# Optimization experiments

Measured on AMD Instinct MI355X. Metric: run time of the kernel, lower is better.

Reference implementation:

```python
import jax, jax.numpy as jnp
import numpy as np

B, C_IN, C_OUT, H, W, K = 8, 64, 64, 64, 64, 9
T = H * W  # 4096 tokens
EPS = 1e-12  # F.normalize eps


def setup_inputs() -> dict:
    key = jax.random.key(0)
    ks = jax.random.split(key, 7)
    x = jax.random.normal(ks[0], (B, C_IN, H, W), dtype=jnp.float32)
    Wq = jax.random.normal(ks[1], (T, T), dtype=jnp.float32) * 0.02
    Wk = jax.random.normal(ks[2], (T, T), dtype=jnp.float32) * 0.02
    Wv = jax.random.normal(ks[3], (T, T), dtype=jnp.float32) * 0.02
    Wo = jax.random.normal(ks[4], (T, T), dtype=jnp.float32) * 0.02
    conv_w = jax.random.normal(ks[5], (C_OUT, C_IN, K), dtype=jnp.float32) * 0.05
    conv_b = jax.random.normal(ks[6], (C_OUT,), dtype=jnp.float32) * 0.01
    return {"x": x, "Wq": Wq, "Wk": Wk, "Wv": Wv, "Wo": Wo,
            "conv_w": conv_w, "conv_b": conv_b}


def reference(x, Wq, Wk, Wv, Wo, conv_w, conv_b):
    Bq, Cc, Hh, Ww = x.shape
    Tt = Hh * Ww
    xf = x.reshape(Bq, Cc, Tt)  # flatten(start_dim=2)
    # nn.Linear over the token (last) dim: y[...,s] = sum_t x[...,t] * W[s,t]
    q = jnp.einsum('bct,st->bcs', xf, Wq)
    k = jnp.einsum('bct,st->bcs', xf, Wk)
    v = jnp.einsum('bct,st->bcs', xf, Wv)
    # cosine similarity over channel dim (dim=1), clamp to >= 0
    kn = k / jnp.maximum(jnp.linalg.norm(k, axis=1, keepdims=True), EPS)
    qn = q / jnp.maximum(jnp.linalg.norm(q, axis=1, keepdims=True), EPS)
    sim = jnp.clip(jnp.einsum('bct,bcs->bts', kn, qn), 0.0, None)  # [B,T,T]
    # top-K most similar neighbors per token (largest=True for similarity)
    _, idx = jax.lax.top_k(sim, K)  # [B,T,K] int32
    # gather neighbor values: prime[b,c,t,j] = v[b,c,idx[b,t,j]]
    gather = jax.vmap(lambda vv, ii: vv[:, ii])  # vv:[C,T], ii:[T,K] -> [C,T,K]
    prime = gather(v, idx).reshape(Bq, Cc, Tt * K)
    # Conv1d(kernel=K, stride=K, padding=0): aggregates each K-neighbor group
    out = jax.lax.conv_general_dilated(
        prime, conv_w, window_strides=(K,), padding='VALID',
        dimension_numbers=('NCH', 'OIH', 'NCH'))  # [B,C_OUT,T]
    out = out + conv_b[None, :, None]
    out = jnp.einsum('bct,st->bcs', out, Wo)  # w_o over token dim
    return out.reshape(Bq, conv_w.shape[0], Hh, Ww)
```

## Files before the change

kernel.cpp:

```cpp
#include <hip/hip_runtime.h>

#define T4096 4096
#define CH 64
typedef unsigned long long u64;

__global__ __launch_bounds__(512) void gemm_qkv(
    const float* __restrict__ X,
    const float* __restrict__ Wq, const float* __restrict__ Wk, const float* __restrict__ Wv,
    float* __restrict__ QT, float* __restrict__ KT, float* __restrict__ VT)
{
    const float* W = (blockIdx.z == 0) ? Wq : (blockIdx.z == 1) ? Wk : Wv;
    float*       O = (blockIdx.z == 0) ? QT : (blockIdx.z == 1) ? KT : VT;
    const int b  = blockIdx.y;
    const int s0 = blockIdx.x * 128;

    __shared__ float As[64][132];
    __shared__ float Bs[64][68];

    const int tid = threadIdx.x;
    const int tx = tid & 15;   const int c0 = tx * 4;
    const int my = tid >> 4;   const int m0 = my * 4;
    const int lr = tid >> 3;
    const int lk = (tid & 7) * 4;
    const int sw = lk;

    float acc[4][4];
#pragma unroll
    for (int i = 0; i < 4; ++i)
#pragma unroll
        for (int j = 0; j < 4; ++j) acc[i][j] = 0.f;

    const float* Xb = X + (size_t)b * CH * T4096;

    for (int k0 = 0; k0 < T4096; k0 += 64) {
#pragma unroll
        for (int kk = 0; kk < 2; ++kk) {
            const int kb = 32 * kk + lk;
#pragma unroll
            for (int p = 0; p < 2; ++p) {
                int row = lr + 64 * p;
                float4 v = *(const float4*)(W + (size_t)(s0 + row) * T4096 + k0 + kb);
                int col = row ^ sw;
                As[kb + 0][col] = v.x; As[kb + 1][col] = v.y;
                As[kb + 2][col] = v.z; As[kb + 3][col] = v.w;
            }
            {
                int row = lr;
                float4 v = *(const float4*)(Xb + (size_t)row * T4096 + k0 + kb);
                int col = row ^ sw;
                Bs[kb + 0][col] = v.x; Bs[kb + 1][col] = v.y;
                Bs[kb + 2][col] = v.z; Bs[kb + 3][col] = v.w;
            }
        }
        __syncthreads();
#pragma unroll
        for (int k = 0; k < 64; ++k) {
            const int swk = k & 28;
            float4 a  = *(const float4*)&As[k][m0 ^ swk];
            float4 bv = *(const float4*)&Bs[k][c0 ^ swk];
            float am[4] = {a.x, a.y, a.z, a.w};
            float bn[4] = {bv.x, bv.y, bv.z, bv.w};
#pragma unroll
            for (int i = 0; i < 4; ++i)
#pragma unroll
                for (int j = 0; j < 4; ++j) acc[i][j] = fmaf(am[i], bn[j], acc[i][j]);
        }
        __syncthreads();
    }
    if (blockIdx.z == 0) {
#pragma unroll
        for (int i = 0; i < 4; ++i) {
            int s = s0 + m0 + i;
            *(float4*)(O + ((((size_t)b * 64 + (s >> 6)) * 16 + tx) * 64 + (s & 63)) * 4) =
                make_float4(acc[i][0], acc[i][1], acc[i][2], acc[i][3]);
        }
    } else {
#pragma unroll
        for (int i = 0; i < 4; ++i) {
            *(float4*)(O + ((size_t)b * T4096 + s0 + m0 + i) * CH + c0) =
                make_float4(acc[i][0], acc[i][1], acc[i][2], acc[i][3]);
        }
    }
}

__global__ __launch_bounds__(256) void normalize_qk(float* __restrict__ QT, float* __restrict__ KT)
{
    int gtok = blockIdx.x * 4 + (threadIdx.x >> 6);
    int lane = threadIdx.x & 63;
    bool isQ = (gtok < 8 * T4096);
    int t = gtok & (T4096 - 1);
    int b = (gtok >> 12) & 7;
    float* p;
    if (isQ) p = QT + ((((size_t)b * 64 + (t >> 6)) * 16 + (lane >> 2)) * 64 + (t & 63)) * 4 + (lane & 3);
    else     p = KT + ((size_t)b * T4096 + t) * CH + lane;
    float v = *p;
    float ss = v * v;
#pragma unroll
    for (int off = 32; off; off >>= 1) ss += __shfl_xor(ss, off);
    float n = fmaxf(sqrtf(ss), 1e-12f);
    *p = v / n;
}

__global__ __launch_bounds__(512) void sim_topk(
    const float* __restrict__ Qr, const float* __restrict__ KT, int* __restrict__ IDX)
{
    const int wg = blockIdx.x;
    const int b  = wg & 7;
    const int t0 = (wg >> 3) * 32;

    __shared__ float Kn[32][68];

    const int tid = threadIdx.x;
    const int tx = tid & 31;
    const int ty = tid >> 5;

    {
        int row = tid >> 4; int cc = (tid & 15) * 4;
        *(float4*)&Kn[row][cc] =
            *(const float4*)(KT + ((size_t)b * T4096 + t0 + row) * CH + cc);
    }
    __syncthreads();

    u64 tv[2][9];
#pragma unroll
    for (int r = 0; r < 2; ++r)
#pragma unroll
        for (int q = 0; q < 9; ++q) tv[r][q] = 0ULL;
    u64 thr[2] = {0ULL, 0ULL};
    unsigned thr_hi[2] = {0u, 0u};

    const float* qb0 = Qr + ((size_t)b * 64 * 1024 + tx) * 4;

    for (int it = 0; it < 16; ++it) {
        const float* bp = qb0 + (size_t)(it * 4) * 4096;
        float acc[2][8];
#pragma unroll
        for (int c = 0; c < 8; ++c) { acc[0][c] = 0.f; acc[1][c] = 0.f; }

#pragma unroll 1
        for (int c4g = 0; c4g < 16; ++c4g) {
            float4 qv[8];
#pragma unroll
            for (int cc = 0; cc < 8; ++cc)
                qv[cc] = *(const float4*)(bp + (size_t)(cc >> 1) * 4096
                                             + c4g * 256 + (cc & 1) * 128);
            float4 k0 = *(const float4*)&Kn[ty][c4g * 4];
            float4 k1 = *(const float4*)&Kn[16 + ty][c4g * 4];
#pragma unroll
            for (int cc = 0; cc < 8; ++cc) {
                acc[0][cc] = fmaf(k0.x, qv[cc].x, acc[0][cc]);
                acc[0][cc] = fmaf(k0.y, qv[cc].y, acc[0][cc]);
                acc[0][cc] = fmaf(k0.z, qv[cc].z, acc[0][cc]);
                acc[0][cc] = fmaf(k0.w, qv[cc].w, acc[0][cc]);
                acc[1][cc] = fmaf(k1.x, qv[cc].x, acc[1][cc]);
                acc[1][cc] = fmaf(k1.y, qv[cc].y, acc[1][cc]);
                acc[1][cc] = fmaf(k1.z, qv[cc].z, acc[1][cc]);
                acc[1][cc] = fmaf(k1.w, qv[cc].w, acc[1][cc]);
            }
        }

        bool ins = false;
        const int sb = it * 256 + tx;
#pragma unroll
        for (int rr = 0; rr < 2; ++rr)
#pragma unroll
            for (int cc = 0; cc < 8; ++cc) {
                float v = fmaxf(acc[rr][cc], 0.f);
                unsigned vb = __float_as_uint(v);
                if (vb >= thr_hi[rr]) {
                    int s = sb + 32 * cc;
                    u64 key = ((u64)vb << 32) | (u64)(4095 - s);
                    if (key > thr[rr]) {
                        u64 cv = key;
#pragma unroll
                        for (int p = 0; p < 9; ++p) {
                            u64 t  = tv[rr][p];
                            bool g = cv > t;
                            tv[rr][p] = g ? cv : t;
                            cv        = g ? t  : cv;
                        }
                        ins = true;
                    }
                }
            }
        if (__any(ins)) {
#pragma unroll
            for (int r = 0; r < 2; ++r) {
                u64 m = tv[r][8];
#pragma unroll
                for (int msk = 1; msk < 32; msk <<= 1) {
                    u64 o = __shfl_xor(m, msk);
                    if (o > m) m = o;
                }
                thr[r] = m;
                thr_hi[r] = (unsigned)(m >> 32);
            }
        }
    }

#pragma unroll
    for (int rr = 0; rr < 2; ++rr) {
        u64 mv[9];
#pragma unroll
        for (int q = 0; q < 9; ++q) mv[q] = tv[rr][q];
        const int outrow = t0 + rr * 16 + ty;
        int* dst = IDX + ((size_t)b * T4096 + outrow) * 9;
        for (int sel = 0; sel < 9; ++sel) {
            u64 bk = mv[0]; int bl = tx;
#pragma unroll
            for (int m = 1; m < 32; m <<= 1) {
                u64 ok = __shfl_xor(bk, m);
                int ol = __shfl_xor(bl, m);
                if (ok > bk) { bk = ok; bl = ol; }
            }
            if (tx == 0) dst[sel] = 4095 - (int)(unsigned)bk;
            if (tx == bl) {
#pragma unroll
                for (int q = 0; q < 8; ++q) mv[q] = mv[q + 1];
                mv[8] = 0ULL;
            }
        }
    }
}

__global__ void transpose_w(const float* __restrict__ cw, float* __restrict__ wT3)
{
    int idx = blockIdx.x * 256 + threadIdx.x;
    if (idx >= 64 * 64 * 9) return;
    int q   = idx & 3;
    int o   = (idx >> 2) & 63;
    int i4g = (idx >> 8) & 15;
    int j   = idx >> 12;
    wT3[idx] = cw[o * 576 + (i4g * 4 + q) * 9 + j];
}

__global__ __launch_bounds__(256) void gather_conv(
    const float* __restrict__ VT, const int* __restrict__ IDX,
    const float* __restrict__ wT3, const float* __restrict__ conv_b,
    float* __restrict__ out1)
{
    const int b  = blockIdx.y;
    const int w  = threadIdx.x >> 6;
    const int o  = threadIdx.x & 63;
    const int t0 = (blockIdx.x * 4 + w) * 4;

    __shared__ float vv[4][4][9][64];
    __shared__ int   nb[4][36];

    if (o < 36) nb[w][o] = IDX[((size_t)b * T4096 + t0) * 9 + o];
    __syncthreads();

#pragma unroll
    for (int tok = 0; tok < 4; ++tok)
#pragma unroll
        for (int j = 0; j < 9; ++j) {
            int n = nb[w][tok * 9 + j];
            vv[w][tok][j][o] = VT[((size_t)b * T4096 + n) * CH + o];
        }
    __syncthreads();

    float cb = conv_b[o];
    float a0 = cb, a1 = cb, a2 = cb, a3 = cb;
    for (int j = 0; j < 9; ++j) {
#pragma unroll
        for (int i4 = 0; i4 < 16; ++i4) {
            float4 w4 = *(const float4*)(wT3 + (((size_t)j * 16 + i4) * 64 + o) * 4);
            float4 v0 = *(const float4*)&vv[w][0][j][i4 * 4];
            float4 v1 = *(const float4*)&vv[w][1][j][i4 * 4];
            float4 v2 = *(const float4*)&vv[w][2][j][i4 * 4];
            float4 v3 = *(const float4*)&vv[w][3][j][i4 * 4];
            a0 = fmaf(v0.x, w4.x, a0); a0 = fmaf(v0.y, w4.y, a0); a0 = fmaf(v0.z, w4.z, a0); a0 = fmaf(v0.w, w4.w, a0);
            a1 = fmaf(v1.x, w4.x, a1); a1 = fmaf(v1.y, w4.y, a1); a1 = fmaf(v1.z, w4.z, a1); a1 = fmaf(v1.w, w4.w, a1);
            a2 = fmaf(v2.x, w4.x, a2); a2 = fmaf(v2.y, w4.y, a2); a2 = fmaf(v2.z, w4.z, a2); a2 = fmaf(v2.w, w4.w, a2);
            a3 = fmaf(v3.x, w4.x, a3); a3 = fmaf(v3.y, w4.y, a3); a3 = fmaf(v3.z, w4.z, a3); a3 = fmaf(v3.w, w4.w, a3);
        }
    }
    out1[((size_t)b * T4096 + t0 + 0) * CH + o] = a0;
    out1[((size_t)b * T4096 + t0 + 1) * CH + o] = a1;
    out1[((size_t)b * T4096 + t0 + 2) * CH + o] = a2;
    out1[((size_t)b * T4096 + t0 + 3) * CH + o] = a3;
}

__global__ __launch_bounds__(256) void gemm_out(
    const float* __restrict__ out1, const float* __restrict__ Wo, float* __restrict__ Out)
{
    const int b  = blockIdx.y;
    const int s0 = blockIdx.x * 64;
    __shared__ float As[64][68];
    __shared__ float Bs[64][68];
    const int tid = threadIdx.x;
    const int tx = tid & 15;  const int sl = tx * 4;
    const int my = tid >> 4;  const int c0 = my * 4;
    const int lk = (tid & 7) * 4;
    const int sw = lk;

    float acc[4][4];
#pragma unroll
    for (int i = 0; i < 4; ++i)
#pragma unroll
        for (int j = 0; j < 4; ++j) acc[i][j] = 0.f;

    for (int k0 = 0; k0 < T4096; k0 += 64) {
        {
            int r  = tid >> 2;
            int cL = (tid & 3) * 16;
            const float* src = out1 + ((size_t)b * T4096 + k0 + r) * CH + cL;
#pragma unroll
            for (int q = 0; q < 4; ++q)
                *(float4*)&As[r][cL + 4 * q] = *(const float4*)(src + 4 * q);
        }
#pragma unroll
        for (int kk = 0; kk < 2; ++kk) {
            const int kb = 32 * kk + lk;
#pragma unroll
            for (int p = 0; p < 2; ++p) {
                int row = (tid >> 3) + 32 * p;
                float4 v = *(const float4*)(Wo + (size_t)(s0 + row) * T4096 + k0 + kb);
                int col = row ^ sw;
                Bs[kb + 0][col] = v.x; Bs[kb + 1][col] = v.y;
                Bs[kb + 2][col] = v.z; Bs[kb + 3][col] = v.w;
            }
        }
        __syncthreads();
#pragma unroll
        for (int k = 0; k < 64; ++k) {
            const int swk = k & 28;
            float4 a  = *(const float4*)&As[k][c0];
            float4 bv = *(const float4*)&Bs[k][sl ^ swk];
            float av[4] = {a.x, a.y, a.z, a.w};
            float bn[4] = {bv.x, bv.y, bv.z, bv.w};
#pragma unroll
            for (int i = 0; i < 4; ++i)
#pragma unroll
                for (int j = 0; j < 4; ++j) acc[i][j] = fmaf(av[i], bn[j], acc[i][j]);
        }
        __syncthreads();
    }
#pragma unroll
    for (int i = 0; i < 4; ++i) {
        float* dst = Out + ((size_t)b * CH + c0 + i) * T4096 + s0 + sl;
        *(float4*)dst = make_float4(acc[i][0], acc[i][1], acc[i][2], acc[i][3]);
    }
}

extern "C" void kernel_launch(void* const* d_in, const int* in_sizes, int n_in,
                              void* d_out, int out_size, void* d_ws, size_t ws_size,
                              hipStream_t stream)
{
    const float* x  = (const float*)d_in[0];
    const float* Wq = (const float*)d_in[1];
    const float* Wk = (const float*)d_in[2];
    const float* Wv = (const float*)d_in[3];
    const float* Wo = (const float*)d_in[4];
    const float* cw = (const float*)d_in[5];
    const float* cb = (const float*)d_in[6];
    float* Out = (float*)d_out;

    char* ws = (char*)d_ws;
    float* QT   = (float*)(ws);
    float* KT   = (float*)(ws + (size_t)8  * 1024 * 1024);
    float* VT   = (float*)(ws + (size_t)16 * 1024 * 1024);
    int*   IDXb = (int*)  (ws + (size_t)24 * 1024 * 1024);
    float* wT3  = (float*)(ws + (size_t)26 * 1024 * 1024);
    float* out1 = QT;

    gemm_qkv<<<dim3(32, 8, 3), dim3(512), 0, stream>>>(x, Wq, Wk, Wv, QT, KT, VT);
    normalize_qk<<<dim3(16384), dim3(256), 0, stream>>>(QT, KT);
    sim_topk<<<dim3(1024), dim3(512), 0, stream>>>(QT, KT, IDXb);
    transpose_w<<<dim3(144), dim3(256), 0, stream>>>(cw, wT3);
    gather_conv<<<dim3(256, 8), dim3(256), 0, stream>>>(VT, IDXb, wT3, cb, out1);
    gemm_out<<<dim3(64, 8), dim3(256), 0, stream>>>(out1, Wo, Out);
}
```

Before: 1.618 ms.

## Fuse Q/K normalization into QKV GEMM, use packed FMA, restructure sim_topk

Computes the per-token channel L2 norm inside the QKV GEMM epilogue with wave shuffles and writes normalized Q (now channel-major) and K directly, which removes the separate normalize kernel launch and its read-modify-write pass. All three GEMM-like loops switch to 2-wide vector FMAs so the compiler can emit packed FP32 FMA instructions. sim_topk reads the new contiguous Q layout with 8 consecutive tokens per thread and adds a max-based early reject before the per-element top-k insertion. The key index is masked to 16 bits on extraction. This adds shuffles and divisions in the GEMM epilogue and changes the memory access pattern in sim_topk.

```diff
diff --git a/kernel.cpp b/kernel.cpp
--- a/kernel.cpp
+++ b/kernel.cpp
@@ -3,14 +3,15 @@
 #define T4096 4096
 #define CH 64
 typedef unsigned long long u64;
+typedef float v2f __attribute__((ext_vector_type(2)));
 
 __global__ __launch_bounds__(512) void gemm_qkv(
     const float* __restrict__ X,
     const float* __restrict__ Wq, const float* __restrict__ Wk, const float* __restrict__ Wv,
-    float* __restrict__ QT, float* __restrict__ KT, float* __restrict__ VT)
+    float* __restrict__ QC, float* __restrict__ KT, float* __restrict__ VT)
 {
     const float* W = (blockIdx.z == 0) ? Wq : (blockIdx.z == 1) ? Wk : Wv;
-    float*       O = (blockIdx.z == 0) ? QT : (blockIdx.z == 1) ? KT : VT;
+    float*       O = (blockIdx.z == 0) ? QC : (blockIdx.z == 1) ? KT : VT;
     const int b  = blockIdx.y;
     const int s0 = blockIdx.x * 128;
 
@@ -24,11 +25,9 @@
     const int lk = (tid & 7) * 4;
     const int sw = lk;
 
-    float acc[4][4];
-#pragma unroll
-    for (int i = 0; i < 4; ++i)
-#pragma unroll
-        for (int j = 0; j < 4; ++j) acc[i][j] = 0.f;
+    v2f acc2[4][2];
+#pragma unroll
+    for (int i = 0; i < 4; ++i) { acc2[i][0] = (v2f)0.f; acc2[i][1] = (v2f)0.f; }
 
     const float* Xb = X + (size_t)b * CH * T4096;
 
@@ -58,51 +57,75 @@
             const int swk = k & 28;
             float4 a  = *(const float4*)&As[k][m0 ^ swk];
             float4 bv = *(const float4*)&Bs[k][c0 ^ swk];
+            v2f b0 = {bv.x, bv.y};
+            v2f b1 = {bv.z, bv.w};
             float am[4] = {a.x, a.y, a.z, a.w};
-            float bn[4] = {bv.x, bv.y, bv.z, bv.w};
-#pragma unroll
-            for (int i = 0; i < 4; ++i)
-#pragma unroll
-                for (int j = 0; j < 4; ++j) acc[i][j] = fmaf(am[i], bn[j], acc[i][j]);
+#pragma unroll
+            for (int i = 0; i < 4; ++i) {
+                v2f as = {am[i], am[i]};
+                acc2[i][0] = __builtin_elementwise_fma(as, b0, acc2[i][0]);
+                acc2[i][1] = __builtin_elementwise_fma(as, b1, acc2[i][1]);
+            }
         }
         __syncthreads();
     }
-    if (blockIdx.z == 0) {
-#pragma unroll
-        for (int i = 0; i < 4; ++i) {
-            int s = s0 + m0 + i;
-            *(float4*)(O + ((((size_t)b * 64 + (s >> 6)) * 16 + tx) * 64 + (s & 63)) * 4) =
-                make_float4(acc[i][0], acc[i][1], acc[i][2], acc[i][3]);
-        }
-    } else {
+
+    if (blockIdx.z == 2) {
 #pragma unroll
         for (int i = 0; i < 4; ++i) {
             *(float4*)(O + ((size_t)b * T4096 + s0 + m0 + i) * CH + c0) =
-                make_float4(acc[i][0], acc[i][1], acc[i][2], acc[i][3]);
-        }
-    }
-}
-
-__global__ __launch_bounds__(256) void normalize_qk(float* __restrict__ QT, float* __restrict__ KT)
-{
-    int gtok = blockIdx.x * 4 + (threadIdx.x >> 6);
-    int lane = threadIdx.x & 63;
-    bool isQ = (gtok < 8 * T4096);
-    int t = gtok & (T4096 - 1);
-    int b = (gtok >> 12) & 7;
-    float* p;
-    if (isQ) p = QT + ((((size_t)b * 64 + (t >> 6)) * 16 + (lane >> 2)) * 64 + (t & 63)) * 4 + (lane & 3);
-    else     p = KT + ((size_t)b * T4096 + t) * CH + lane;
-    float v = *p;
-    float ss = v * v;
-#pragma unroll
-    for (int off = 32; off; off >>= 1) ss += __shfl_xor(ss, off);
-    float n = fmaxf(sqrtf(ss), 1e-12f);
-    *p = v / n;
+                make_float4(acc2[i][0].x, acc2[i][0].y, acc2[i][1].x, acc2[i][1].y);
+        }
+        return;
+    }
+
+    float nrm[4];
+#pragma unroll
+    for (int i = 0; i < 4; ++i) {
+        float p0 = acc2[i][0].x * acc2[i][0].x;
+        float p1 = acc2[i][0].y * acc2[i][0].y;
+        float p2 = acc2[i][1].x * acc2[i][1].x;
+        float p3 = acc2[i][1].y * acc2[i][1].y;
+        p0 += __shfl_xor(p0, 8); p1 += __shfl_xor(p1, 8);
+        p2 += __shfl_xor(p2, 8); p3 += __shfl_xor(p3, 8);
+        p0 += __shfl_xor(p0, 4); p1 += __shfl_xor(p1, 4);
+        p2 += __shfl_xor(p2, 4); p3 += __shfl_xor(p3, 4);
+        p0 += __shfl_xor(p0, 2); p1 += __shfl_xor(p1, 2);
+        p2 += __shfl_xor(p2, 2); p3 += __shfl_xor(p3, 2);
+        p0 += __shfl_xor(p0, 1); p1 += __shfl_xor(p1, 1);
+        p2 += __shfl_xor(p2, 1); p3 += __shfl_xor(p3, 1);
+        float r0 = p0 + p2;
+        float r1 = p1 + p3;
+        float ss = r0 + r1;
+        nrm[i] = fmaxf(sqrtf(ss), 1e-12f);
+    }
+
+    if (blockIdx.z == 0) {
+        float vj[4][4];
+#pragma unroll
+        for (int i = 0; i < 4; ++i) {
+            vj[0][i] = acc2[i][0].x / nrm[i];
+            vj[1][i] = acc2[i][0].y / nrm[i];
+            vj[2][i] = acc2[i][1].x / nrm[i];
+            vj[3][i] = acc2[i][1].y / nrm[i];
+        }
+#pragma unroll
+        for (int j = 0; j < 4; ++j) {
+            *(float4*)(O + ((size_t)b * CH + c0 + j) * T4096 + s0 + m0) =
+                make_float4(vj[j][0], vj[j][1], vj[j][2], vj[j][3]);
+        }
+    } else {
+#pragma unroll
+        for (int i = 0; i < 4; ++i) {
+            *(float4*)(O + ((size_t)b * T4096 + s0 + m0 + i) * CH + c0) =
+                make_float4(acc2[i][0].x / nrm[i], acc2[i][0].y / nrm[i],
+                            acc2[i][1].x / nrm[i], acc2[i][1].y / nrm[i]);
+        }
+    }
 }
 
 __global__ __launch_bounds__(512) void sim_topk(
-    const float* __restrict__ Qr, const float* __restrict__ KT, int* __restrict__ IDX)
+    const float* __restrict__ QC, const float* __restrict__ KT, int* __restrict__ IDX)
 {
     const int wg = blockIdx.x;
     const int b  = wg & 7;
@@ -129,60 +152,76 @@
     u64 thr[2] = {0ULL, 0ULL};
     unsigned thr_hi[2] = {0u, 0u};
 
-    const float* qb0 = Qr + ((size_t)b * 64 * 1024 + tx) * 4;
-
-    for (int it = 0; it < 16; ++it) {
-        const float* bp = qb0 + (size_t)(it * 4) * 4096;
-        float acc[2][8];
-#pragma unroll
-        for (int c = 0; c < 8; ++c) { acc[0][c] = 0.f; acc[1][c] = 0.f; }
-
-#pragma unroll 1
+    const float* qcb = QC + (size_t)b * CH * T4096 + tx * 8;
+
+    for (int chk = 0; chk < 16; ++chk) {
+        const int cbase = chk * 256;
+        const float* qk = qcb + cbase;
+
+        v2f acc2[2][4];
+#pragma unroll
+        for (int m = 0; m < 4; ++m) { acc2[0][m] = (v2f)0.f; acc2[1][m] = (v2f)0.f; }
+
+#pragma unroll 2
         for (int c4g = 0; c4g < 16; ++c4g) {
-            float4 qv[8];
-#pragma unroll
-            for (int cc = 0; cc < 8; ++cc)
-                qv[cc] = *(const float4*)(bp + (size_t)(cc >> 1) * 4096
-                                             + c4g * 256 + (cc & 1) * 128);
-            float4 k0 = *(const float4*)&Kn[ty][c4g * 4];
-            float4 k1 = *(const float4*)&Kn[16 + ty][c4g * 4];
-#pragma unroll
-            for (int cc = 0; cc < 8; ++cc) {
-                acc[0][cc] = fmaf(k0.x, qv[cc].x, acc[0][cc]);
-                acc[0][cc] = fmaf(k0.y, qv[cc].y, acc[0][cc]);
-                acc[0][cc] = fmaf(k0.z, qv[cc].z, acc[0][cc]);
-                acc[0][cc] = fmaf(k0.w, qv[cc].w, acc[0][cc]);
-                acc[1][cc] = fmaf(k1.x, qv[cc].x, acc[1][cc]);
-                acc[1][cc] = fmaf(k1.y, qv[cc].y, acc[1][cc]);
-                acc[1][cc] = fmaf(k1.z, qv[cc].z, acc[1][cc]);
-                acc[1][cc] = fmaf(k1.w, qv[cc].w, acc[1][cc]);
+            float4 kv0 = *(const float4*)&Kn[ty][c4g * 4];
+            float4 kv1 = *(const float4*)&Kn[16 + ty][c4g * 4];
+            float km0[4] = {kv0.x, kv0.y, kv0.z, kv0.w};
+            float km1[4] = {kv1.x, kv1.y, kv1.z, kv1.w};
+#pragma unroll
+            for (int cs = 0; cs < 4; ++cs) {
+                const float* qp = qk + (size_t)(c4g * 4 + cs) * T4096;
+                float4 qa = *(const float4*)(qp);
+                float4 qb = *(const float4*)(qp + 4);
+                v2f q0 = {qa.x, qa.y};
+                v2f q1 = {qa.z, qa.w};
+                v2f q2 = {qb.x, qb.y};
+                v2f q3 = {qb.z, qb.w};
+                v2f k0 = {km0[cs], km0[cs]};
+                v2f k1 = {km1[cs], km1[cs]};
+                acc2[0][0] = __builtin_elementwise_fma(k0, q0, acc2[0][0]);
+                acc2[0][1] = __builtin_elementwise_fma(k0, q1, acc2[0][1]);
+                acc2[0][2] = __builtin_elementwise_fma(k0, q2, acc2[0][2]);
+                acc2[0][3] = __builtin_elementwise_fma(k0, q3, acc2[0][3]);
+                acc2[1][0] = __builtin_elementwise_fma(k1, q0, acc2[1][0]);
+                acc2[1][1] = __builtin_elementwise_fma(k1, q1, acc2[1][1]);
+                acc2[1][2] = __builtin_elementwise_fma(k1, q2, acc2[1][2]);
+                acc2[1][3] = __builtin_elementwise_fma(k1, q3, acc2[1][3]);
             }
         }
 
         bool ins = false;
-        const int sb = it * 256 + tx;
-#pragma unroll
-        for (int rr = 0; rr < 2; ++rr)
-#pragma unroll
-            for (int cc = 0; cc < 8; ++cc) {
-                float v = fmaxf(acc[rr][cc], 0.f);
-                unsigned vb = __float_as_uint(v);
-                if (vb >= thr_hi[rr]) {
-                    int s = sb + 32 * cc;
-                    u64 key = ((u64)vb << 32) | (u64)(4095 - s);
-                    if (key > thr[rr]) {
-                        u64 cv = key;
-#pragma unroll
-                        for (int p = 0; p < 9; ++p) {
-                            u64 t  = tv[rr][p];
-                            bool g = cv > t;
-                            tv[rr][p] = g ? cv : t;
-                            cv        = g ? t  : cv;
+#pragma unroll
+        for (int rr = 0; rr < 2; ++rr) {
+            v2f m01 = __builtin_elementwise_max(acc2[rr][0], acc2[rr][1]);
+            v2f m23 = __builtin_elementwise_max(acc2[rr][2], acc2[rr][3]);
+            v2f mm  = __builtin_elementwise_max(m01, m23);
+            float vmax = fmaxf(fmaxf(mm.x, mm.y), 0.f);
+            if (!(vmax < __uint_as_float(thr_hi[rr]))) {
+#pragma unroll
+                for (int m = 0; m < 4; ++m)
+#pragma unroll
+                    for (int h = 0; h < 2; ++h) {
+                        float v = fmaxf(h ? acc2[rr][m].y : acc2[rr][m].x, 0.f);
+                        unsigned vb = __float_as_uint(v);
+                        if (vb >= thr_hi[rr]) {
+                            int s = cbase + tx * 8 + 2 * m + h;
+                            u64 key = ((u64)vb << 32) | (u64)(4095 - s);
+                            if (key > thr[rr]) {
+                                u64 cv = key;
+#pragma unroll
+                                for (int p = 0; p < 9; ++p) {
+                                    u64 t  = tv[rr][p];
+                                    bool g = cv > t;
+                                    tv[rr][p] = g ? cv : t;
+                                    cv       = g ? t  : cv;
+                                }
+                                ins = true;
+                            }
                         }
-                        ins = true;
                     }
-                }
-            }
+            }
+        }
         if (__any(ins)) {
 #pragma unroll
             for (int r = 0; r < 2; ++r) {
@@ -213,7 +252,7 @@
                 int ol = __shfl_xor(bl, m);
                 if (ok > bk) { bk = ok; bl = ol; }
             }
-            if (tx == 0) dst[sel] = 4095 - (int)(unsigned)bk;
+            if (tx == 0) dst[sel] = 4095 - (int)(unsigned)(bk & 0xffffULL);
             if (tx == bl) {
 #pragma unroll
                 for (int q = 0; q < 8; ++q) mv[q] = mv[q + 1];
@@ -294,11 +333,9 @@
     const int lk = (tid & 7) * 4;
     const int sw = lk;
 
-    float acc[4][4];
-#pragma unroll
-    for (int i = 0; i < 4; ++i)
-#pragma unroll
-        for (int j = 0; j < 4; ++j) acc[i][j] = 0.f;
+    v2f acc2[4][2];
+#pragma unroll
+    for (int i = 0; i < 4; ++i) { acc2[i][0] = (v2f)0.f; acc2[i][1] = (v2f)0.f; }
 
     for (int k0 = 0; k0 < T4096; k0 += 64) {
         {
@@ -327,19 +364,22 @@
             const int swk = k & 28;
             float4 a  = *(const float4*)&As[k][c0];
             float4 bv = *(const float4*)&Bs[k][sl ^ swk];
+            v2f b0 = {bv.x, bv.y};
+            v2f b1 = {bv.z, bv.w};
             float av[4] = {a.x, a.y, a.z, a.w};
-            float bn[4] = {bv.x, bv.y, bv.z, bv.w};
-#pragma unroll
-            for (int i = 0; i < 4; ++i)
-#pragma unroll
-                for (int j = 0; j < 4; ++j) acc[i][j] = fmaf(av[i], bn[j], acc[i][j]);
+#pragma unroll
+            for (int i = 0; i < 4; ++i) {
+                v2f as = {av[i], av[i]};
+                acc2[i][0] = __builtin_elementwise_fma(as, b0, acc2[i][0]);
+                acc2[i][1] = __builtin_elementwise_fma(as, b1, acc2[i][1]);
+            }
         }
         __syncthreads();
     }
 #pragma unroll
     for (int i = 0; i < 4; ++i) {
         float* dst = Out + ((size_t)b * CH + c0 + i) * T4096 + s0 + sl;
-        *(float4*)dst = make_float4(acc[i][0], acc[i][1], acc[i][2], acc[i][3]);
+        *(float4*)dst = make_float4(acc2[i][0].x, acc2[i][0].y, acc2[i][1].x, acc2[i][1].y);
     }
 }
 
@@ -357,16 +397,15 @@
     float* Out = (float*)d_out;
 
     char* ws = (char*)d_ws;
-    float* QT   = (float*)(ws);
+    float* QC   = (float*)(ws);
     float* KT   = (float*)(ws + (size_t)8  * 1024 * 1024);
     float* VT   = (float*)(ws + (size_t)16 * 1024 * 1024);
     int*   IDXb = (int*)  (ws + (size_t)24 * 1024 * 1024);
     float* wT3  = (float*)(ws + (size_t)26 * 1024 * 1024);
-    float* out1 = QT;
-
-    gemm_qkv<<<dim3(32, 8, 3), dim3(512), 0, stream>>>(x, Wq, Wk, Wv, QT, KT, VT);
-    normalize_qk<<<dim3(16384), dim3(256), 0, stream>>>(QT, KT);
-    sim_topk<<<dim3(1024), dim3(512), 0, stream>>>(QT, KT, IDXb);
+    float* out1 = QC;
+
+    gemm_qkv<<<dim3(32, 8, 3), dim3(512), 0, stream>>>(x, Wq, Wk, Wv, QC, KT, VT);
+    sim_topk<<<dim3(1024), dim3(512), 0, stream>>>(QC, KT, IDXb);
     transpose_w<<<dim3(144), dim3(256), 0, stream>>>(cw, wT3);
     gather_conv<<<dim3(256, 8), dim3(256), 0, stream>>>(VT, IDXb, wT3, cb, out1);
     gemm_out<<<dim3(64, 8), dim3(256), 0, stream>>>(out1, Wo, Out);
```

After: 1.592 ms. Within noise of the previous version (-1.6%).
